# Performance work log

Measured on AMD Instinct MI355X. Metric: run time of the kernel, lower is better.

## Reference

```python
import jax, jax.numpy as jnp
import numpy as np

NUM_TOKENS = 1024  # codebook size (n_embed)
CODE_DIM = 256     # embedding_dim
BETA = 0.25


def setup_inputs() -> dict:
    key = jax.random.key(0)
    k1, k2 = jax.random.split(key)
    z = jax.random.normal(k1, (64, 512, CODE_DIM), dtype=jnp.float32)
    weight = jax.random.normal(k2, (NUM_TOKENS, CODE_DIM), dtype=jnp.float32)
    return {"z": z, "weight": weight}


def reference(z, weight):
    # z: [B, T, D]; weight: [K, D]
    z_flat = z.reshape(-1, CODE_DIM)                       # [N, D]
    # squared euclidean distances: ||z||^2 + ||w||^2 - 2 z.w
    d = (jnp.sum(z_flat ** 2, axis=1, keepdims=True)
         + jnp.sum(weight ** 2, axis=1)
         - 2.0 * jnp.matmul(z_flat, weight.T))             # [N, K]
    min_encoding_indices = jnp.argmin(d, axis=1)           # [N]
    z_q = weight[min_encoding_indices].reshape(z.shape)    # gather

    # perplexity from mean one-hot usage (avoid materializing one-hot via bincount)
    counts = jnp.bincount(min_encoding_indices, length=NUM_TOKENS)
    e_mean = counts.astype(z.dtype) / z_flat.shape[0]
    perplexity = jnp.exp(-jnp.sum(e_mean * jnp.log(e_mean + 1e-10)))

    # commitment loss (codebook is EMA-updated, so z_q is detached)
    loss = BETA * jnp.mean((jax.lax.stop_gradient(z_q) - z) ** 2)
    # straight-through estimator
    z_q_st = z + jax.lax.stop_gradient(z_q - z)
    return (loss, z_q_st, min_encoding_indices, perplexity)
```

## Files before the change

kernel.cpp:

```cpp
#include <hip/hip_runtime.h>

#define N_TOKENS 32768
#define K_CODES  1024
#define DIM      256
#define BETA     0.25f

typedef unsigned long long u64;
typedef _Float16 half8 __attribute__((ext_vector_type(8)));
typedef float floatx4 __attribute__((ext_vector_type(4)));

__global__ void init_kernel(const float* __restrict__ w, float* __restrict__ wn,
                            int* __restrict__ counts, u64* __restrict__ keys,
                            _Float16* __restrict__ whiG, _Float16* __restrict__ wloG) {
    int k = blockIdx.x;
    int lane = threadIdx.x;
    float4 v = *(const float4*)(w + (size_t)k * DIM + lane * 4);
    float vals[4] = {v.x, v.y, v.z, v.w};
    float s = 0.f;
    #pragma unroll
    for (int e = 0; e < 4; e++) {
        s += vals[e] * vals[e];
        _Float16 h = (_Float16)vals[e];
        whiG[k * DIM + lane * 4 + e] = h;
        wloG[k * DIM + lane * 4 + e] = (_Float16)(vals[e] - (float)h);
    }
    #pragma unroll
    for (int off = 32; off; off >>= 1) s += __shfl_down(s, off);
    if (lane == 0) { wn[k] = s; counts[k] = 0; }
    if (lane < 32) keys[k * 32 + lane] = ~0ull;
}

__global__ __launch_bounds__(256, 2) void argmin_kernel(
    const float* __restrict__ z, const _Float16* __restrict__ whiG,
    const _Float16* __restrict__ wloG, const float* __restrict__ wn,
    u64* __restrict__ keys)
{
    constexpr int ZS = 40;
    __shared__ _Float16 zhi[128 * ZS], zlo[128 * ZS];
    __shared__ _Float16 whi[256 * ZS], wlo[256 * ZS];
    __shared__ float wns[256];

    const int tid  = threadIdx.x;
    const int lane = tid & 63;
    const int wid  = tid >> 6;
    const int wm   = wid >> 1;
    const int wq   = wid & 1;
    const int t_   = blockIdx.x & 255;
    const int q    = blockIdx.x >> 8;
    const int tok0  = t_ * 128;
    const int kbase = q * 256;

    wns[tid] = wn[kbase + tid];

    floatx4 acc[4][8];
    #pragma unroll
    for (int i = 0; i < 4; i++)
        #pragma unroll
        for (int j = 0; j < 8; j++)
            acc[i][j] = (floatx4){0.f, 0.f, 0.f, 0.f};

    const int r0 = tid >> 2;
    const int g0 = tid & 3;

    for (int dt = 0; dt < 8; ++dt) {
        const int d0 = dt * 32;
        __syncthreads();

        #pragma unroll
        for (int s = 0; s < 2; s++) {
            int t = r0 + s * 64;
            const float* p = z + (size_t)(tok0 + t) * DIM + d0 + g0 * 8;
            float4 a = *(const float4*)p;
            float4 b = *(const float4*)(p + 4);
            float vals[8] = {a.x, a.y, a.z, a.w, b.x, b.y, b.z, b.w};
            half8 hv, lv;
            #pragma unroll
            for (int e = 0; e < 8; e++) {
                _Float16 h = (_Float16)vals[e];
                hv[e] = h;
                lv[e] = (_Float16)(vals[e] - (float)h);
            }
            *(half8*)&zhi[t * ZS + g0 * 8] = hv;
            *(half8*)&zlo[t * ZS + g0 * 8] = lv;
        }
        #pragma unroll
        for (int s = 0; s < 4; s++) {
            int t = r0 + s * 64;
            size_t goff = (size_t)(kbase + t) * DIM + d0 + g0 * 8;
            *(half8*)&whi[t * ZS + g0 * 8] = *(const half8*)&whiG[goff];
            *(half8*)&wlo[t * ZS + g0 * 8] = *(const half8*)&wloG[goff];
        }
        __syncthreads();

        const int koff = (lane >> 4) * 8;
        half8 ah[4], al[4];
        #pragma unroll
        for (int i = 0; i < 4; i++) {
            int off = (wm * 64 + i * 16 + (lane & 15)) * ZS + koff;
            ah[i] = *(const half8*)&zhi[off];
            al[i] = *(const half8*)&zlo[off];
        }
        #pragma unroll
        for (int j = 0; j < 8; j++) {
            int off = (wq * 128 + j * 16 + (lane & 15)) * ZS + koff;
            half8 bh = *(const half8*)&whi[off];
            half8 bl = *(const half8*)&wlo[off];
            #pragma unroll
            for (int i = 0; i < 4; i++) {
                acc[i][j] = __builtin_amdgcn_mfma_f32_16x16x32_f16(ah[i], bh, acc[i][j], 0, 0, 0);
                acc[i][j] = __builtin_amdgcn_mfma_f32_16x16x32_f16(ah[i], bl, acc[i][j], 0, 0, 0);
                acc[i][j] = __builtin_amdgcn_mfma_f32_16x16x32_f16(al[i], bh, acc[i][j], 0, 0, 0);
            }
        }
    }

    #pragma unroll
    for (int i = 0; i < 4; i++) {
        #pragma unroll
        for (int r = 0; r < 4; r++) {
            float bv = 3.4e38f; int bi = 0;
            #pragma unroll
            for (int j = 0; j < 8; j++) {
                int cl = wq * 128 + j * 16 + (lane & 15);
                float dist = wns[cl] - 2.0f * acc[i][j][r];
                if (dist < bv) { bv = dist; bi = kbase + cl; }
            }
            unsigned uu = __float_as_uint(bv);
            unsigned ss = (uu & 0x80000000u) ? ~uu : (uu | 0x80000000u);
            u64 key = ((u64)ss << 32) | (unsigned)bi;
            #pragma unroll
            for (int m = 1; m < 16; m <<= 1) {
                u64 o = __shfl_xor(key, m);
                if (o < key) key = o;
            }
            if ((lane & 15) == 0) {
                int token = tok0 + wm * 64 + i * 16 + (lane >> 4) * 4 + r;
                atomicMin(&keys[token], key);
            }
        }
    }
}

__global__ void gather_loss_kernel(const float* __restrict__ z,
                                   const float* __restrict__ w,
                                   const u64* __restrict__ keys,
                                   float* __restrict__ zq_out,
                                   float* __restrict__ idxf,
                                   int* __restrict__ counts,
                                   float* __restrict__ partials)
{
    __shared__ float red[4];
    int tid = threadIdx.x;
    int lane = tid & 63;
    int wid = blockIdx.x * 4 + (tid >> 6);
    float s = 0.0f;
    #pragma unroll
    for (int it = 0; it < 4; it++) {
        int tok = wid + it * 8192;
        u64 key = 0;
        if (lane == 0) key = keys[tok];
        key = __shfl(key, 0);
        int k = (int)(unsigned)(key & 0xFFFFFFFFull);
        float4 wv = *(const float4*)(w + (size_t)k * DIM + lane * 4);
        float4 zv = *(const float4*)(z + (size_t)tok * DIM + lane * 4);
        *(float4*)(zq_out + (size_t)tok * DIM + lane * 4) = wv;
        float dx = wv.x - zv.x, dy = wv.y - zv.y, dz = wv.z - zv.z, dw = wv.w - zv.w;
        s += dx * dx + dy * dy + dz * dz + dw * dw;
        if (lane == 0) {
            idxf[tok] = (float)k;
            atomicAdd(&counts[k], 1);
        }
    }
    #pragma unroll
    for (int off = 32; off; off >>= 1) s += __shfl_down(s, off);
    if (lane == 0) red[tid >> 6] = s;
    __syncthreads();
    if (tid == 0)
        partials[blockIdx.x] = red[0] + red[1] + red[2] + red[3];
}

__global__ void finalize_kernel(const int* __restrict__ counts,
                                const float* __restrict__ partials,
                                float* __restrict__ loss_out,
                                float* __restrict__ ppl_out)
{
    __shared__ float redE[16], redL[16];
    int tid = threadIdx.x;
    float e = (float)counts[tid] * (1.0f / (float)N_TOKENS);
    float t = -e * logf(e + 1e-10f);
    float p = partials[tid] + partials[tid + 1024];
    #pragma unroll
    for (int off = 32; off; off >>= 1) {
        t += __shfl_down(t, off);
        p += __shfl_down(p, off);
    }
    if ((tid & 63) == 0) { redE[tid >> 6] = t; redL[tid >> 6] = p; }
    __syncthreads();
    if (tid == 0) {
        float se = 0.0f, sl = 0.0f;
        #pragma unroll
        for (int i = 0; i < 16; i++) { se += redE[i]; sl += redL[i]; }
        *ppl_out = expf(se);
        *loss_out = BETA * sl / (float)((size_t)N_TOKENS * DIM);
    }
}

extern "C" void kernel_launch(void* const* d_in, const int* in_sizes, int n_in,
                              void* d_out, int out_size, void* d_ws, size_t ws_size,
                              hipStream_t stream) {
    const float* z = (const float*)d_in[0];
    const float* w = (const float*)d_in[1];
    float* out = (float*)d_out;

    float* loss_out = out;
    float* zq_out   = out + 1;
    float* idxf     = out + 1 + (size_t)N_TOKENS * DIM;
    float* ppl_out  = out + (out_size - 1);

    float* wn       = (float*)d_ws;
    int*   counts   = (int*)d_ws + 1024;
    float* partials = (float*)d_ws + 2048;
    u64*   keys     = (u64*)((char*)d_ws + 16384);
    _Float16* whiG  = (_Float16*)((char*)d_ws + 16384 + (size_t)N_TOKENS * 8);
    _Float16* wloG  = whiG + (size_t)K_CODES * DIM;

    init_kernel<<<K_CODES, 64, 0, stream>>>(w, wn, counts, keys, whiG, wloG);
    argmin_kernel<<<4 * 256, 256, 0, stream>>>(z, whiG, wloG, wn, keys);
    gather_loss_kernel<<<2048, 256, 0, stream>>>(z, w, keys, zq_out, idxf, counts, partials);
    finalize_kernel<<<1, 1024, 0, stream>>>(counts, partials, loss_out, ppl_out);
}
```

Measured before the change: 158.2 us.

## Prefetch next z/codebook chunk into registers during MFMA compute

The argmin kernel now loads the next d-chunk of z and the split-half codebook from global memory into registers before running the MFMA work on the current chunk. The staged values are written to shared memory after a barrier, so global latency can overlap with compute. The codebook norms move from shared memory into per-thread registers. In exchange this raises register pressure under the launch bound of 2 blocks per SM and adds an extra barrier per iteration. The index mask in the gather kernel is also changed.

```diff
diff --git a/kernel.cpp b/kernel.cpp
--- a/kernel.cpp
+++ b/kernel.cpp
@@ -38,7 +38,6 @@
     constexpr int ZS = 40;
     __shared__ _Float16 zhi[128 * ZS], zlo[128 * ZS];
     __shared__ _Float16 whi[256 * ZS], wlo[256 * ZS];
-    __shared__ float wns[256];
 
     const int tid  = threadIdx.x;
     const int lane = tid & 63;
@@ -50,7 +49,10 @@
     const int tok0  = t_ * 128;
     const int kbase = q * 256;
 
-    wns[tid] = wn[kbase + tid];
+    float wnr[8];
+    #pragma unroll
+    for (int j = 0; j < 8; j++)
+        wnr[j] = wn[kbase + wq * 128 + j * 16 + (lane & 15)];
 
     floatx4 acc[4][8];
     #pragma unroll
@@ -62,23 +64,36 @@
     const int r0 = tid >> 2;
     const int g0 = tid & 3;
 
-    for (int dt = 0; dt < 8; ++dt) {
+    float zr[16];
+    half8 wh[4], wl[4];
+
+    auto load_chunk = [&](int dt) {
         const int d0 = dt * 32;
-        __syncthreads();
-
+        #pragma unroll
+        for (int s = 0; s < 2; s++) {
+            const float* p = z + (size_t)(tok0 + r0 + s * 64) * DIM + d0 + g0 * 8;
+            float4 a = *(const float4*)p;
+            float4 b = *(const float4*)(p + 4);
+            zr[s * 8 + 0] = a.x; zr[s * 8 + 1] = a.y; zr[s * 8 + 2] = a.z; zr[s * 8 + 3] = a.w;
+            zr[s * 8 + 4] = b.x; zr[s * 8 + 5] = b.y; zr[s * 8 + 6] = b.z; zr[s * 8 + 7] = b.w;
+        }
+        #pragma unroll
+        for (int s = 0; s < 4; s++) {
+            size_t goff = (size_t)(kbase + r0 + s * 64) * DIM + d0 + g0 * 8;
+            wh[s] = *(const half8*)&whiG[goff];
+            wl[s] = *(const half8*)&wloG[goff];
+        }
+    };
+    auto write_chunk = [&]() {
         #pragma unroll
         for (int s = 0; s < 2; s++) {
             int t = r0 + s * 64;
-            const float* p = z + (size_t)(tok0 + t) * DIM + d0 + g0 * 8;
-            float4 a = *(const float4*)p;
-            float4 b = *(const float4*)(p + 4);
-            float vals[8] = {a.x, a.y, a.z, a.w, b.x, b.y, b.z, b.w};
             half8 hv, lv;
             #pragma unroll
             for (int e = 0; e < 8; e++) {
-                _Float16 h = (_Float16)vals[e];
+                _Float16 h = (_Float16)zr[s * 8 + e];
                 hv[e] = h;
-                lv[e] = (_Float16)(vals[e] - (float)h);
+                lv[e] = (_Float16)(zr[s * 8 + e] - (float)h);
             }
             *(half8*)&zhi[t * ZS + g0 * 8] = hv;
             *(half8*)&zlo[t * ZS + g0 * 8] = lv;
@@ -86,11 +101,17 @@
         #pragma unroll
         for (int s = 0; s < 4; s++) {
             int t = r0 + s * 64;
-            size_t goff = (size_t)(kbase + t) * DIM + d0 + g0 * 8;
-            *(half8*)&whi[t * ZS + g0 * 8] = *(const half8*)&whiG[goff];
-            *(half8*)&wlo[t * ZS + g0 * 8] = *(const half8*)&wloG[goff];
-        }
-        __syncthreads();
+            *(half8*)&whi[t * ZS + g0 * 8] = wh[s];
+            *(half8*)&wlo[t * ZS + g0 * 8] = wl[s];
+        }
+    };
+
+    load_chunk(0);
+    write_chunk();
+    __syncthreads();
+
+    for (int dt = 0; dt < 8; ++dt) {
+        if (dt < 7) load_chunk(dt + 1);
 
         const int koff = (lane >> 4) * 8;
         half8 ah[4], al[4];
@@ -112,6 +133,9 @@
                 acc[i][j] = __builtin_amdgcn_mfma_f32_16x16x32_f16(al[i], bh, acc[i][j], 0, 0, 0);
             }
         }
+        __syncthreads();
+        if (dt < 7) write_chunk();
+        __syncthreads();
     }
 
     #pragma unroll
@@ -122,7 +146,7 @@
             #pragma unroll
             for (int j = 0; j < 8; j++) {
                 int cl = wq * 128 + j * 16 + (lane & 15);
-                float dist = wns[cl] - 2.0f * acc[i][j][r];
+                float dist = wnr[j] - 2.0f * acc[i][j][r];
                 if (dist < bv) { bv = dist; bi = kbase + cl; }
             }
             unsigned uu = __float_as_uint(bv);
@@ -160,7 +184,7 @@
         u64 key = 0;
         if (lane == 0) key = keys[tok];
         key = __shfl(key, 0);
-        int k = (int)(unsigned)(key & 0xFFFFFFFFull);
+        int k = (int)(key & (u64)(K_CODES - 1));
         float4 wv = *(const float4*)(w + (size_t)k * DIM + lane * 4);
         float4 zv = *(const float4*)(z + (size_t)tok * DIM + lane * 4);
         *(float4*)(zq_out + (size_t)tok * DIM + lane * 4) = wv;
```

Measured after the change: 161.4 us. 2.0% more time.
